# Kernel tuning notes

Hardware: AMD Instinct MI355X
Metric: run time of the kernel (lower is better)

Reference implementation:

```python
import jax, jax.numpy as jnp
import numpy as np

B, L, DM, H, DK, DV = 4, 1024, 1024, 16, 64, 64


def setup_inputs() -> dict:
    key = jax.random.key(0)
    ks = jax.random.split(key, 9)
    s = 0.02
    q = jax.random.normal(ks[0], (B, L, DM), jnp.float32)
    k = jax.random.normal(ks[1], (B, L, DM), jnp.float32)
    v = jax.random.normal(ks[2], (B, L, DM), jnp.float32)
    # causal mask: True = masked out
    attn_mask = jnp.broadcast_to(jnp.triu(jnp.ones((L, L), bool), k=1), (B, L, L))
    w_q = jax.random.normal(ks[3], (DM, H * DK), jnp.float32) * s
    w_k = jax.random.normal(ks[4], (DM, H * DK), jnp.float32) * s
    w_v = jax.random.normal(ks[5], (DM, H * DV), jnp.float32) * s
    w_o = jax.random.normal(ks[6], (H * DV, DM), jnp.float32) * s
    ln_g = jnp.ones((DM,), jnp.float32)
    ln_b = jnp.zeros((DM,), jnp.float32)
    return {"q": q, "k": k, "v": v, "w_q": w_q, "w_k": w_k, "w_v": w_v,
            "w_o": w_o, "ln_g": ln_g, "ln_b": ln_b,
            "attn_mask": attn_mask, "n_head": H}


def _mha(q, k, v, w_q, w_k, w_v, w_o, ln_g, ln_b, attn_mask, n_head):
    b, lq, dm = q.shape
    lk = k.shape[1]
    d_k = w_q.shape[1] // n_head
    d_v = w_v.shape[1] // n_head
    temper = jnp.asarray(np.sqrt(dm), q.dtype)  # NOTE: sqrt(d_model), as in source
    residual = q
    # faithful to source: flat .view reshape (b, l, h*d) -> (b*h, l, d), NO transpose
    qh = (q @ w_q).reshape(b * n_head, lq, d_k)
    kh = (k @ w_k).reshape(b * n_head, lk, d_k)
    vh = (v @ w_v).reshape(b * n_head, lk, d_v)
    attn = jnp.einsum('bqd,bkd->bqk', qh, kh) / temper  # (b*h, lq, lk)
    mask_r = jnp.tile(attn_mask, (n_head, 1, 1))
    attn = jnp.where(mask_r, -jnp.inf, attn)
    attn = jax.nn.softmax(attn, axis=-1)
    out = jnp.einsum('bqk,bkd->bqd', attn, vh)  # (b*h, lq, d_v)
    out = out.reshape(b, lq, n_head * d_v)
    out = out @ w_o + residual  # dropout = identity (eval)
    mu = jnp.mean(out, axis=-1, keepdims=True)
    var = jnp.mean(jnp.square(out - mu), axis=-1, keepdims=True)
    out = (out - mu) * jax.lax.rsqrt(var + 1e-6) * ln_g + ln_b
    return out, attn


def reference(q, k, v, w_q, w_k, w_v, w_o, ln_g, ln_b, attn_mask, n_head):
    return _mha(q, k, v, w_q, w_k, w_v, w_o, ln_g, ln_b, attn_mask, n_head)
```

## Files before the change

kernel.cpp:

```cpp
#include <hip/hip_runtime.h>
#include <stdint.h>

typedef unsigned short u16;
typedef __attribute__((ext_vector_type(8))) short bf16x8;
typedef __attribute__((ext_vector_type(4))) float f32x4;
typedef __attribute__((ext_vector_type(4))) unsigned short us4;

#define MFMA_BF16(a, b, c) __builtin_amdgcn_mfma_f32_16x16x32_bf16((a), (b), (c), 0, 0, 0)

__device__ __forceinline__ u16 f2bf(float f) {
  uint32_t u = __builtin_bit_cast(uint32_t, f);
  u += 0x7fffu + ((u >> 16) & 1u);
  return (u16)(u >> 16);
}

__device__ __forceinline__ void async_copy16(void* lds, const void* g) {
  __builtin_amdgcn_global_load_lds(
      (const __attribute__((address_space(1))) unsigned int*)g,
      (__attribute__((address_space(3))) unsigned int*)lds, 16, 0, 0);
}

__global__ __launch_bounds__(256) void k_pre(const float* __restrict__ q,
                                             const float* __restrict__ k,
                                             const float* __restrict__ v,
                                             const float* __restrict__ w0,
                                             const float* __restrict__ w1,
                                             const float* __restrict__ w2,
                                             const float* __restrict__ w3,
                                             us4* __restrict__ qkvb,
                                             u16* __restrict__ wT) {
  __shared__ float t[32][33];
  int bid = blockIdx.x;
  int tid = threadIdx.x;
  if (bid < 12288) {
    int z = bid >> 12;
    const float4* src = (z == 0) ? (const float4*)q : (z == 1) ? (const float4*)k : (const float4*)v;
    int i = (bid & 4095) * 256 + tid;
    float4 val = src[i];
    us4 o;
    o[0] = f2bf(val.x); o[1] = f2bf(val.y); o[2] = f2bf(val.z); o[3] = f2bf(val.w);
    qkvb[(size_t)z * 1048576 + i] = o;
  } else {
    int w = bid - 12288;
    int z = w >> 10, r_ = w & 1023;
    int bx = r_ & 31, by = r_ >> 5;
    const float* W = (z == 0) ? w0 : (z == 1) ? w1 : (z == 2) ? w2 : w3;
    u16* WT = wT + (size_t)z * 1048576;
    int c = tid & 31, r0 = tid >> 5;
#pragma unroll
    for (int i = 0; i < 4; ++i) {
      int r = r0 + i * 8;
      t[r][c] = W[(size_t)(by * 32 + r) * 1024 + bx * 32 + c];
    }
    __syncthreads();
#pragma unroll
    for (int i = 0; i < 4; ++i) {
      int r = r0 + i * 8;
      WT[(size_t)(bx * 32 + r) * 1024 + by * 32 + c] = f2bf(t[c][r]);
    }
  }
}

__global__ __launch_bounds__(256) void k_vtrans(const u16* __restrict__ VP, u16* __restrict__ VT) {
  int jt = blockIdx.x;
  int bh = blockIdx.y;
  __shared__ u16 t[64][65];
  int tid = threadIdx.x;
  const u16* src = VP + (size_t)bh * 65536 + (size_t)jt * 64 * 64;
#pragma unroll
  for (int i = 0; i < 16; ++i) {
    int e = tid + i * 256;
    t[e >> 6][e & 63] = src[e];
  }
  __syncthreads();
  u16* dst = VT + (size_t)bh * 65536 + jt * 64;
#pragma unroll
  for (int i = 0; i < 16; ++i) {
    int e = tid + i * 256;
    int d = e >> 6, j = e & 63;
    dst[(size_t)d * 1024 + j] = t[j][d];
  }
}

__global__ __launch_bounds__(256) void k_gemm_bt(const u16* __restrict__ A,
                                                 const u16* __restrict__ BT,
                                                 u16* __restrict__ Cb, float* __restrict__ Cf,
                                                 const float* __restrict__ res,
                                                 int N, int K, int mode, int wgrp) {
  __shared__ __align__(16) u16 SM[4][4096];
  int bm, bn;
  {
    int wg = blockIdx.x + blockIdx.y * gridDim.x;
    int per = gridDim.y >> 3;
    int xcd = wg & 7;
    int idx = wg >> 3;
    bm = xcd * per + (idx % per);
    bn = idx / per;
  }
  int tid = threadIdx.x;
  int wave = tid >> 6, lane = tid & 63;
  int wr = wave >> 1, wc = wave & 1;
  int fl = lane & 15, fg = lane >> 4;
  f32x4 acc[4][4] = {};

  const char* Abase = (const char*)(A + (size_t)bm * 128 * K);
  const char* Bbase = (const char*)(BT + (wgrp ? (size_t)(bm >> 5) * 1048576 : 0) +
                                    (size_t)bn * 128 * K);
  int off = wave * 1024 + lane * 16;

#define GSTAGE(buf, kt)                                                              \
  {                                                                                  \
    _Pragma("unroll") for (int is = 0; is < 2; ++is) {                               \
      int o = is * 4096 + off;                                                       \
      int row = o >> 6, cb = o & 63;                                                 \
      async_copy16((char*)SM[buf] + is * 4096 + wave * 1024,                         \
                   Abase + (size_t)row * (K * 2) + (kt) * 2 + cb);                   \
      async_copy16((char*)SM[2 + (buf)] + is * 4096 + wave * 1024,                   \
                   Bbase + (size_t)row * (K * 2) + (kt) * 2 + cb);                   \
    }                                                                                \
  }

  GSTAGE(0, 0);
  __syncthreads();
  int cur = 0;
  for (int kt = 0; kt < K; kt += 32) {
    if (kt + 32 < K) GSTAGE(cur ^ 1, kt + 32);
    bf16x8 af[4], bfr[4];
#pragma unroll
    for (int m = 0; m < 4; ++m)
      af[m] = *(const bf16x8*)((const char*)SM[cur] + (wr * 64 + m * 16 + fl) * 64 + fg * 16);
#pragma unroll
    for (int n = 0; n < 4; ++n)
      bfr[n] = *(const bf16x8*)((const char*)SM[2 + cur] + (wc * 64 + n * 16 + fl) * 64 + fg * 16);
#pragma unroll
    for (int m = 0; m < 4; ++m)
#pragma unroll
      for (int n = 0; n < 4; ++n)
        acc[m][n] = MFMA_BF16(af[m], bfr[n], acc[m][n]);
    __syncthreads();
    cur ^= 1;
  }
#undef GSTAGE

  float* EP = (float*)&SM[0][0] + wave * 2048;
  int colbase = bn * 128 + wc * 64;
#pragma unroll
  for (int m = 0; m < 4; ++m) {
    int rowbase = bm * 128 + wr * 64 + m * 16;
#pragma unroll
    for (int n = 0; n < 4; ++n)
#pragma unroll
      for (int r = 0; r < 4; ++r)
        EP[(fg * 4 + r) * 68 + n * 16 + fl] = acc[m][n][r];
    if (mode) {
#pragma unroll
      for (int j = 0; j < 4; ++j) {
        int row = (lane >> 4) + 4 * j;
        int colf = (lane & 15) * 4;
        float4 val = *(const float4*)(&EP[row * 68 + colf]);
        size_t gidx = (size_t)(rowbase + row) * N + colbase + colf;
        float4 rr = *(const float4*)(res + gidx);
        val.x += rr.x; val.y += rr.y; val.z += rr.z; val.w += rr.w;
        *(float4*)(Cf + gidx) = val;
      }
    } else {
#pragma unroll
      for (int j = 0; j < 2; ++j) {
        int row = (lane >> 3) + 8 * j;
        int colf = (lane & 7) * 8;
        const float* s = &EP[row * 68 + colf];
        us4 lo, hi;
#pragma unroll
        for (int i = 0; i < 4; ++i) { lo[i] = f2bf(s[i]); hi[i] = f2bf(s[4 + i]); }
        u16* d = Cb + (size_t)(rowbase + row) * N + colbase + colf;
        *(us4*)d = lo;
        *(us4*)(d + 4) = hi;
      }
    }
  }
}

__global__ __launch_bounds__(256) void k_attn(const u16* __restrict__ QP,
                                              const u16* __restrict__ KP,
                                              const u16* __restrict__ VT,
                                              float* __restrict__ attn,
                                              u16* __restrict__ AO) {
  int bh = blockIdx.x;
  int qb = 15 - blockIdx.y;
  int tid = threadIdx.x;
  int wave = tid >> 6, lane = tid & 63;
  int fl = lane & 15, fg = lane >> 4;
  int qw = qb * 64 + wave * 16;

  const u16* Qb = QP + (size_t)bh * 65536;
  const char* Kbyte = (const char*)(KP + (size_t)bh * 65536);
  const u16* Vb = VT + (size_t)bh * 65536;
  float* Ab = attn + (size_t)bh * 1048576;

  __shared__ __align__(16) u16 Ks[2][4096];
  __shared__ __align__(16) float Ps[4][16][36];
  __shared__ __align__(16) u16 Pt[4][16][64];

#define KSTAGE(buf, jt)                                                                 \
  {                                                                                     \
    _Pragma("unroll") for (int c2 = 0; c2 < 2; ++c2) {                                  \
      int o = c2 * 4096 + wave * 1024 + lane * 16;                                      \
      int row = o >> 7, col = o & 127;                                                  \
      async_copy16((char*)Ks[buf] + c2 * 4096 + wave * 1024,                            \
                   Kbyte + (size_t)((jt) * 64 + row) * 128 + (col ^ ((row & 7) << 4))); \
    }                                                                                   \
  }

  bf16x8 qf0 = *(const bf16x8*)(Qb + (size_t)(qw + fl) * 64 + fg * 8);
  bf16x8 qf1 = *(const bf16x8*)(Qb + (size_t)(qw + fl) * 64 + 32 + fg * 8);

  float den[4] = {0.f, 0.f, 0.f, 0.f};

  KSTAGE(0, 0);
  __syncthreads();
  int cur = 0;
  for (int jt = 0; jt <= qb; ++jt) {
    if (jt < qb) KSTAGE(cur ^ 1, jt + 1);
    int j0 = jt * 64;
    f32x4 c[4] = {};
#pragma unroll
    for (int n = 0; n < 4; ++n) {
      int r = n * 16 + fl;
      bf16x8 k0 = *(const bf16x8*)((const char*)Ks[cur] + r * 128 + ((fg * 16) ^ ((r & 7) << 4)));
      bf16x8 k1 = *(const bf16x8*)((const char*)Ks[cur] + r * 128 + ((64 + fg * 16) ^ ((r & 7) << 4)));
      c[n] = MFMA_BF16(qf0, k0, c[n]);
      c[n] = MFMA_BF16(qf1, k1, c[n]);
    }
#pragma unroll
    for (int r = 0; r < 4; ++r) {
      int row = qw + fg * 4 + r;
      float sum = 0.f;
#pragma unroll
      for (int n = 0; n < 4; ++n) {
        int col = j0 + n * 16 + fl;
        sum += (col > row) ? 0.f : __expf(c[n][r] * 0.03125f);
      }
#pragma unroll
      for (int o2 = 1; o2 < 16; o2 <<= 1) sum += __shfl_xor(sum, o2);
      den[r] += sum;
    }
    __syncthreads();
    cur ^= 1;
  }

  float invden[4];
#pragma unroll
  for (int r = 0; r < 4; ++r) invden[r] = 1.0f / den[r];

  f32x4 oacc[4] = {};

  KSTAGE(0, 0);
  __syncthreads();
  cur = 0;
  for (int jt = 0; jt <= qb; ++jt) {
    if (jt < qb) KSTAGE(cur ^ 1, jt + 1);
    int j0 = jt * 64;
    f32x4 c[4] = {};
#pragma unroll
    for (int n = 0; n < 4; ++n) {
      int r = n * 16 + fl;
      bf16x8 k0 = *(const bf16x8*)((const char*)Ks[cur] + r * 128 + ((fg * 16) ^ ((r & 7) << 4)));
      bf16x8 k1 = *(const bf16x8*)((const char*)Ks[cur] + r * 128 + ((64 + fg * 16) ^ ((r & 7) << 4)));
      c[n] = MFMA_BF16(qf0, k0, c[n]);
      c[n] = MFMA_BF16(qf1, k1, c[n]);
    }
    float pv_[4][4];
#pragma unroll
    for (int r = 0; r < 4; ++r) {
      int row = qw + fg * 4 + r;
#pragma unroll
      for (int n = 0; n < 4; ++n) {
        int col = j0 + n * 16 + fl;
        pv_[n][r] = (col > row) ? 0.f : __expf(c[n][r] * 0.03125f) * invden[r];
      }
    }
#pragma unroll
    for (int t = 0; t < 2; ++t) {
#pragma unroll
      for (int n2 = 0; n2 < 2; ++n2)
#pragma unroll
        for (int r = 0; r < 4; ++r)
          Ps[wave][fg * 4 + r][n2 * 16 + fl] = pv_[t * 2 + n2][r];
#pragma unroll
      for (int i = 0; i < 2; ++i) {
        int idx = i * 64 + lane;
        int r16 = idx >> 3, f4 = idx & 7;
        float4 val = *(const float4*)(&Ps[wave][r16][f4 * 4]);
        *(float4*)(Ab + (size_t)(qw + r16) * 1024 + j0 + t * 32 + f4 * 4) = val;
      }
    }
#pragma unroll
    for (int r = 0; r < 4; ++r)
#pragma unroll
      for (int n = 0; n < 4; ++n)
        Pt[wave][fg * 4 + r][n * 16 + fl] = f2bf(pv_[n][r]);
    bf16x8 pa0 = *(const bf16x8*)(&Pt[wave][fl][fg * 8]);
    bf16x8 pa1 = *(const bf16x8*)(&Pt[wave][fl][32 + fg * 8]);
#pragma unroll
    for (int n = 0; n < 4; ++n) {
      const u16* vp = Vb + (size_t)(n * 16 + fl) * 1024 + j0;
      bf16x8 v0 = *(const bf16x8*)(vp + fg * 8);
      bf16x8 v1 = *(const bf16x8*)(vp + 32 + fg * 8);
      oacc[n] = MFMA_BF16(pa0, v0, oacc[n]);
      oacc[n] = MFMA_BF16(pa1, v1, oacc[n]);
    }
    __syncthreads();
    cur ^= 1;
  }
#undef KSTAGE

  float4 z; z.x = 0.f; z.y = 0.f; z.z = 0.f; z.w = 0.f;
  for (int jt = qb + 1; jt < 16; ++jt) {
    int j0 = jt * 64;
#pragma unroll
    for (int i = 0; i < 4; ++i) {
      int idx = i * 64 + lane;
      int r16 = idx >> 4, f4 = idx & 15;
      *(float4*)(Ab + (size_t)(qw + r16) * 1024 + j0 + f4 * 4) = z;
    }
  }

#pragma unroll
  for (int n = 0; n < 4; ++n)
#pragma unroll
    for (int r = 0; r < 4; ++r)
      Pt[wave][fg * 4 + r][n * 16 + fl] = f2bf(oacc[n][r]);
#pragma unroll
  for (int j = 0; j < 2; ++j) {
    int row = (lane >> 3) + 8 * j;
    int colf = (lane & 7) * 8;
    bf16x8 val = *(const bf16x8*)(&Pt[wave][row][colf]);
    *(bf16x8*)(AO + (size_t)bh * 65536 + (size_t)(qw + row) * 64 + colf) = val;
  }
}

__global__ __launch_bounds__(256) void k_lnorm(float* __restrict__ io,
                                               const float* __restrict__ g,
                                               const float* __restrict__ b) {
  int row = blockIdx.x, tid = threadIdx.x;
  float* p = io + (size_t)row * 1024 + tid * 4;
  float4 x = *(const float4*)p;
  float s1 = x.x + x.y + x.z + x.w;
  float s2 = x.x * x.x + x.y * x.y + x.z * x.z + x.w * x.w;
#pragma unroll
  for (int o = 1; o < 64; o <<= 1) {
    s1 += __shfl_xor(s1, o);
    s2 += __shfl_xor(s2, o);
  }
  __shared__ float r1[4], r2[4];
  int wave = tid >> 6;
  if ((tid & 63) == 0) { r1[wave] = s1; r2[wave] = s2; }
  __syncthreads();
  s1 = r1[0] + r1[1] + r1[2] + r1[3];
  s2 = r2[0] + r2[1] + r2[2] + r2[3];
  float mu = s1 * (1.0f / 1024.0f);
  float var = s2 * (1.0f / 1024.0f) - mu * mu;
  float rs = rsqrtf(var + 1e-6f);
  float4 gg = *(const float4*)(g + tid * 4);
  float4 bb = *(const float4*)(b + tid * 4);
  float4 y;
  y.x = (x.x - mu) * rs * gg.x + bb.x;
  y.y = (x.y - mu) * rs * gg.y + bb.y;
  y.z = (x.z - mu) * rs * gg.z + bb.z;
  y.w = (x.w - mu) * rs * gg.w + bb.w;
  *(float4*)p = y;
}

extern "C" void kernel_launch(void* const* d_in, const int* in_sizes, int n_in,
                              void* d_out, int out_size, void* d_ws, size_t ws_size,
                              hipStream_t stream) {
  const float* q = (const float*)d_in[0];
  const float* k = (const float*)d_in[1];
  const float* v = (const float*)d_in[2];
  const float* w_q = (const float*)d_in[3];
  const float* w_k = (const float*)d_in[4];
  const float* w_v = (const float*)d_in[5];
  const float* w_o = (const float*)d_in[6];
  const float* ln_g = (const float*)d_in[7];
  const float* ln_b = (const float*)d_in[8];

  float* out = (float*)d_out;
  float* attnp = out + 4194304;

  char* ws = (char*)d_ws;
  u16* QP = (u16*)(ws);
  u16* VP = (u16*)(ws + (16u << 20));
  u16* VT = (u16*)(ws + (24u << 20));
  u16* AO = (u16*)(ws + (32u << 20));
  u16* wT = (u16*)(ws + (40u << 20));
  u16* KP = QP + 4194304;
  u16* woT = wT + 3145728;

  u16* qkvb = (u16*)attnp;

  k_pre<<<16384, 256, 0, stream>>>(q, k, v, w_q, w_k, w_v, w_o, (us4*)qkvb, wT);

  k_gemm_bt<<<dim3(8, 96), 256, 0, stream>>>(qkvb, wT, QP, nullptr, nullptr, 1024, 1024, 0, 1);

  k_vtrans<<<dim3(16, 64), 256, 0, stream>>>(VP, VT);

  k_attn<<<dim3(64, 16), 256, 0, stream>>>(QP, KP, VT, attnp, AO);

  k_gemm_bt<<<dim3(8, 32), 256, 0, stream>>>(AO, woT, nullptr, out, q, 1024, 1024, 1, 0);

  k_lnorm<<<4096, 256, 0, stream>>>(out, ln_g, ln_b);
}
```

Before: 170.5 us.

## Fuse fp32-to-bf16 input conversion into QKV GEMM and move mask zeroing there

Drops the separate q/k/v fp32-to-bf16 conversion pass. The QKV GEMM now stages fp32 activations into swizzled LDS and converts them to bf16 with packed cvt instructions while loading fragments. Extra blocks in the same QKV launch zero the causal upper triangle of the attention output, work that used to be done at the tail of the attention kernel. The attention kernel also stops staging K through LDS and reads K directly from global memory, removing its barriers. In exchange, the GEMM moves twice as many A bytes through LDS, and the attention kernel relies on uncoalesced direct K reads.

```diff
diff --git a/kernel.cpp b/kernel.cpp
--- a/kernel.cpp
+++ b/kernel.cpp
@@ -20,44 +20,37 @@
       (__attribute__((address_space(3))) unsigned int*)lds, 16, 0, 0);
 }
 
-__global__ __launch_bounds__(256) void k_pre(const float* __restrict__ q,
-                                             const float* __restrict__ k,
-                                             const float* __restrict__ v,
-                                             const float* __restrict__ w0,
-                                             const float* __restrict__ w1,
-                                             const float* __restrict__ w2,
-                                             const float* __restrict__ w3,
-                                             us4* __restrict__ qkvb,
-                                             u16* __restrict__ wT) {
+__device__ __forceinline__ bf16x8 cvt8(f32x4 lo, f32x4 hi) {
+  union { bf16x8 v; uint32_t w[4]; } u;
+  asm("v_cvt_pk_bf16_f32 %0, %1, %2" : "=v"(u.w[0]) : "v"(lo[0]), "v"(lo[1]));
+  asm("v_cvt_pk_bf16_f32 %0, %1, %2" : "=v"(u.w[1]) : "v"(lo[2]), "v"(lo[3]));
+  asm("v_cvt_pk_bf16_f32 %0, %1, %2" : "=v"(u.w[2]) : "v"(hi[0]), "v"(hi[1]));
+  asm("v_cvt_pk_bf16_f32 %0, %1, %2" : "=v"(u.w[3]) : "v"(hi[2]), "v"(hi[3]));
+  return u.v;
+}
+
+__global__ __launch_bounds__(256) void k_wtrans4(const float* __restrict__ w0,
+                                                 const float* __restrict__ w1,
+                                                 const float* __restrict__ w2,
+                                                 const float* __restrict__ w3,
+                                                 u16* __restrict__ dstbase) {
+  const float* W = (blockIdx.z == 0) ? w0 : (blockIdx.z == 1) ? w1
+                   : (blockIdx.z == 2) ? w2 : w3;
+  u16* WT = dstbase + (size_t)blockIdx.z * 1048576;
   __shared__ float t[32][33];
-  int bid = blockIdx.x;
+  int bx = blockIdx.x, by = blockIdx.y;
   int tid = threadIdx.x;
-  if (bid < 12288) {
-    int z = bid >> 12;
-    const float4* src = (z == 0) ? (const float4*)q : (z == 1) ? (const float4*)k : (const float4*)v;
-    int i = (bid & 4095) * 256 + tid;
-    float4 val = src[i];
-    us4 o;
-    o[0] = f2bf(val.x); o[1] = f2bf(val.y); o[2] = f2bf(val.z); o[3] = f2bf(val.w);
-    qkvb[(size_t)z * 1048576 + i] = o;
-  } else {
-    int w = bid - 12288;
-    int z = w >> 10, r_ = w & 1023;
-    int bx = r_ & 31, by = r_ >> 5;
-    const float* W = (z == 0) ? w0 : (z == 1) ? w1 : (z == 2) ? w2 : w3;
-    u16* WT = wT + (size_t)z * 1048576;
-    int c = tid & 31, r0 = tid >> 5;
-#pragma unroll
-    for (int i = 0; i < 4; ++i) {
-      int r = r0 + i * 8;
-      t[r][c] = W[(size_t)(by * 32 + r) * 1024 + bx * 32 + c];
-    }
-    __syncthreads();
-#pragma unroll
-    for (int i = 0; i < 4; ++i) {
-      int r = r0 + i * 8;
-      WT[(size_t)(bx * 32 + r) * 1024 + by * 32 + c] = f2bf(t[c][r]);
-    }
+  int c = tid & 31, r0 = tid >> 5;
+#pragma unroll
+  for (int i = 0; i < 4; ++i) {
+    int r = r0 + i * 8;
+    t[r][c] = W[(size_t)(by * 32 + r) * 1024 + bx * 32 + c];
+  }
+  __syncthreads();
+#pragma unroll
+  for (int i = 0; i < 4; ++i) {
+    int r = r0 + i * 8;
+    WT[(size_t)(bx * 32 + r) * 1024 + by * 32 + c] = f2bf(t[c][r]);
   }
 }
 
@@ -82,56 +75,83 @@
   }
 }
 
-__global__ __launch_bounds__(256) void k_gemm_bt(const u16* __restrict__ A,
-                                                 const u16* __restrict__ BT,
-                                                 u16* __restrict__ Cb, float* __restrict__ Cf,
-                                                 const float* __restrict__ res,
-                                                 int N, int K, int mode, int wgrp) {
-  __shared__ __align__(16) u16 SM[4][4096];
-  int bm, bn;
-  {
-    int wg = blockIdx.x + blockIdx.y * gridDim.x;
-    int per = gridDim.y >> 3;
-    int xcd = wg & 7;
-    int idx = wg >> 3;
-    bm = xcd * per + (idx % per);
-    bn = idx / per;
-  }
+__global__ __launch_bounds__(256) void k_gemm_qkv(const float* __restrict__ q,
+                                                  const float* __restrict__ k,
+                                                  const float* __restrict__ v,
+                                                  const u16* __restrict__ wT,
+                                                  u16* __restrict__ C,
+                                                  float* __restrict__ attnp) {
+  __shared__ __align__(16) float Asm[2][4096];
+  __shared__ __align__(16) u16 Bsm[2][4096];
+  int id = blockIdx.x;
+  int xcd = id & 7, seq = id >> 3;
+  int grp = seq / 7, r7 = seq % 7;
   int tid = threadIdx.x;
+  if (r7 >= 3) {
+    int zid = xcd * 128 + grp * 4 + (r7 - 3);
+    int bh = zid >> 4, qb = zid & 15;
+    int W = 960 - 64 * qb;
+    if (W > 0 && tid * 4 < W) {
+      float* base = attnp + (size_t)bh * 1048576 + (size_t)qb * 65536 + (qb + 1) * 64 + tid * 4;
+      float4 z = {0.f, 0.f, 0.f, 0.f};
+#pragma unroll 8
+      for (int row = 0; row < 64; ++row) *(float4*)(base + row * 1024) = z;
+    }
+    return;
+  }
+  int gi = grp * 3 + r7;
+  int bn = gi & 7;
+  int bm = xcd * 12 + (gi >> 3);
+  int z = bm >> 5;
   int wave = tid >> 6, lane = tid & 63;
   int wr = wave >> 1, wc = wave & 1;
   int fl = lane & 15, fg = lane >> 4;
   f32x4 acc[4][4] = {};
 
-  const char* Abase = (const char*)(A + (size_t)bm * 128 * K);
-  const char* Bbase = (const char*)(BT + (wgrp ? (size_t)(bm >> 5) * 1048576 : 0) +
-                                    (size_t)bn * 128 * K);
-  int off = wave * 1024 + lane * 16;
-
-#define GSTAGE(buf, kt)                                                              \
-  {                                                                                  \
-    _Pragma("unroll") for (int is = 0; is < 2; ++is) {                               \
-      int o = is * 4096 + off;                                                       \
-      int row = o >> 6, cb = o & 63;                                                 \
-      async_copy16((char*)SM[buf] + is * 4096 + wave * 1024,                         \
-                   Abase + (size_t)row * (K * 2) + (kt) * 2 + cb);                   \
-      async_copy16((char*)SM[2 + (buf)] + is * 4096 + wave * 1024,                   \
-                   Bbase + (size_t)row * (K * 2) + (kt) * 2 + cb);                   \
-    }                                                                                \
-  }
-
-  GSTAGE(0, 0);
+  const char* Ab = (const char*)((z == 0 ? q : z == 1 ? k : v) + (size_t)(bm & 31) * 131072);
+  const char* Bb = (const char*)(wT + (size_t)z * 1048576 + (size_t)bn * 131072);
+
+#define ASTAGE(buf, kt)                                                        \
+  {                                                                            \
+    _Pragma("unroll") for (int is = 0; is < 4; ++is) {                         \
+      int o = is * 4096 + wave * 1024 + lane * 16;                             \
+      int row = o >> 7, cb = o & 127;                                          \
+      async_copy16((char*)Asm[buf] + is * 4096 + wave * 1024,                  \
+                   Ab + (size_t)row * 4096 + (kt) * 4 + (cb ^ ((row & 7) << 4))); \
+    }                                                                          \
+  }
+#define BSTAGE(buf, kt)                                                        \
+  {                                                                            \
+    _Pragma("unroll") for (int is = 0; is < 2; ++is) {                         \
+      int o = is * 4096 + wave * 1024 + lane * 16;                             \
+      int row = o >> 6, cb = o & 63;                                           \
+      async_copy16((char*)Bsm[buf] + is * 4096 + wave * 1024,                  \
+                   Bb + (size_t)row * 2048 + (kt) * 2 + cb);                   \
+    }                                                                          \
+  }
+
+  ASTAGE(0, 0);
+  BSTAGE(0, 0);
   __syncthreads();
   int cur = 0;
-  for (int kt = 0; kt < K; kt += 32) {
-    if (kt + 32 < K) GSTAGE(cur ^ 1, kt + 32);
+  for (int kt = 0; kt < 1024; kt += 32) {
+    if (kt + 32 < 1024) {
+      ASTAGE(cur ^ 1, kt + 32);
+      BSTAGE(cur ^ 1, kt + 32);
+    }
     bf16x8 af[4], bfr[4];
 #pragma unroll
-    for (int m = 0; m < 4; ++m)
-      af[m] = *(const bf16x8*)((const char*)SM[cur] + (wr * 64 + m * 16 + fl) * 64 + fg * 16);
+    for (int m = 0; m < 4; ++m) {
+      int R = wr * 64 + m * 16 + fl;
+      const char* ar = (const char*)Asm[cur] + R * 128;
+      int s = (R & 7) << 4;
+      f32x4 lo = *(const f32x4*)(ar + ((fg * 32) ^ s));
+      f32x4 hi = *(const f32x4*)(ar + ((fg * 32 + 16) ^ s));
+      af[m] = cvt8(lo, hi);
+    }
 #pragma unroll
     for (int n = 0; n < 4; ++n)
-      bfr[n] = *(const bf16x8*)((const char*)SM[2 + cur] + (wc * 64 + n * 16 + fl) * 64 + fg * 16);
+      bfr[n] = *(const bf16x8*)((const char*)Bsm[cur] + (wc * 64 + n * 16 + fl) * 64 + fg * 16);
 #pragma unroll
     for (int m = 0; m < 4; ++m)
 #pragma unroll
@@ -140,9 +160,10 @@
     __syncthreads();
     cur ^= 1;
   }
-#undef GSTAGE
-
-  float* EP = (float*)&SM[0][0] + wave * 2048;
+#undef ASTAGE
+#undef BSTAGE
+
+  float* EP = (float*)&Asm[0][0] + wave * 1088;
   int colbase = bn * 128 + wc * 64;
 #pragma unroll
   for (int m = 0; m < 4; ++m) {
@@ -152,30 +173,17 @@
 #pragma unroll
       for (int r = 0; r < 4; ++r)
         EP[(fg * 4 + r) * 68 + n * 16 + fl] = acc[m][n][r];
-    if (mode) {
-#pragma unroll
-      for (int j = 0; j < 4; ++j) {
-        int row = (lane >> 4) + 4 * j;
-        int colf = (lane & 15) * 4;
-        float4 val = *(const float4*)(&EP[row * 68 + colf]);
-        size_t gidx = (size_t)(rowbase + row) * N + colbase + colf;
-        float4 rr = *(const float4*)(res + gidx);
-        val.x += rr.x; val.y += rr.y; val.z += rr.z; val.w += rr.w;
-        *(float4*)(Cf + gidx) = val;
-      }
-    } else {
-#pragma unroll
-      for (int j = 0; j < 2; ++j) {
-        int row = (lane >> 3) + 8 * j;
-        int colf = (lane & 7) * 8;
-        const float* s = &EP[row * 68 + colf];
-        us4 lo, hi;
-#pragma unroll
-        for (int i = 0; i < 4; ++i) { lo[i] = f2bf(s[i]); hi[i] = f2bf(s[4 + i]); }
-        u16* d = Cb + (size_t)(rowbase + row) * N + colbase + colf;
-        *(us4*)d = lo;
-        *(us4*)(d + 4) = hi;
-      }
+#pragma unroll
+    for (int j = 0; j < 2; ++j) {
+      int row = (lane >> 3) + 8 * j;
+      int colf = (lane & 7) * 8;
+      const float* sp = &EP[row * 68 + colf];
+      us4 lo4, hi4;
+#pragma unroll
+      for (int i = 0; i < 4; ++i) { lo4[i] = f2bf(sp[i]); hi4[i] = f2bf(sp[4 + i]); }
+      u16* d = C + (size_t)(rowbase + row) * 1024 + colbase + colf;
+      *(us4*)d = lo4;
+      *(us4*)(d + 4) = hi4;
     }
   }
 }
@@ -193,41 +201,26 @@
   int qw = qb * 64 + wave * 16;
 
   const u16* Qb = QP + (size_t)bh * 65536;
-  const char* Kbyte = (const char*)(KP + (size_t)bh * 65536);
+  const u16* Kb = KP + (size_t)bh * 65536;
   const u16* Vb = VT + (size_t)bh * 65536;
   float* Ab = attn + (size_t)bh * 1048576;
 
-  __shared__ __align__(16) u16 Ks[2][4096];
   __shared__ __align__(16) float Ps[4][16][36];
   __shared__ __align__(16) u16 Pt[4][16][64];
 
-#define KSTAGE(buf, jt)                                                                 \
-  {                                                                                     \
-    _Pragma("unroll") for (int c2 = 0; c2 < 2; ++c2) {                                  \
-      int o = c2 * 4096 + wave * 1024 + lane * 16;                                      \
-      int row = o >> 7, col = o & 127;                                                  \
-      async_copy16((char*)Ks[buf] + c2 * 4096 + wave * 1024,                            \
-                   Kbyte + (size_t)((jt) * 64 + row) * 128 + (col ^ ((row & 7) << 4))); \
-    }                                                                                   \
-  }
-
   bf16x8 qf0 = *(const bf16x8*)(Qb + (size_t)(qw + fl) * 64 + fg * 8);
   bf16x8 qf1 = *(const bf16x8*)(Qb + (size_t)(qw + fl) * 64 + 32 + fg * 8);
 
   float den[4] = {0.f, 0.f, 0.f, 0.f};
 
-  KSTAGE(0, 0);
-  __syncthreads();
-  int cur = 0;
   for (int jt = 0; jt <= qb; ++jt) {
-    if (jt < qb) KSTAGE(cur ^ 1, jt + 1);
     int j0 = jt * 64;
     f32x4 c[4] = {};
 #pragma unroll
     for (int n = 0; n < 4; ++n) {
-      int r = n * 16 + fl;
-      bf16x8 k0 = *(const bf16x8*)((const char*)Ks[cur] + r * 128 + ((fg * 16) ^ ((r & 7) << 4)));
-      bf16x8 k1 = *(const bf16x8*)((const char*)Ks[cur] + r * 128 + ((64 + fg * 16) ^ ((r & 7) << 4)));
+      const u16* kp = Kb + (size_t)(j0 + n * 16 + fl) * 64;
+      bf16x8 k0 = *(const bf16x8*)(kp + fg * 8);
+      bf16x8 k1 = *(const bf16x8*)(kp + 32 + fg * 8);
       c[n] = MFMA_BF16(qf0, k0, c[n]);
       c[n] = MFMA_BF16(qf1, k1, c[n]);
     }
@@ -244,8 +237,6 @@
       for (int o2 = 1; o2 < 16; o2 <<= 1) sum += __shfl_xor(sum, o2);
       den[r] += sum;
     }
-    __syncthreads();
-    cur ^= 1;
   }
 
   float invden[4];
@@ -254,18 +245,14 @@
 
   f32x4 oacc[4] = {};
 
-  KSTAGE(0, 0);
-  __syncthreads();
-  cur = 0;
   for (int jt = 0; jt <= qb; ++jt) {
-    if (jt < qb) KSTAGE(cur ^ 1, jt + 1);
     int j0 = jt * 64;
     f32x4 c[4] = {};
 #pragma unroll
     for (int n = 0; n < 4; ++n) {
-      int r = n * 16 + fl;
-      bf16x8 k0 = *(const bf16x8*)((const char*)Ks[cur] + r * 128 + ((fg * 16) ^ ((r & 7) << 4)));
-      bf16x8 k1 = *(const bf16x8*)((const char*)Ks[cur] + r * 128 + ((64 + fg * 16) ^ ((r & 7) << 4)));
+      const u16* kp = Kb + (size_t)(j0 + n * 16 + fl) * 64;
+      bf16x8 k0 = *(const bf16x8*)(kp + fg * 8);
+      bf16x8 k1 = *(const bf16x8*)(kp + 32 + fg * 8);
       c[n] = MFMA_BF16(qf0, k0, c[n]);
       c[n] = MFMA_BF16(qf1, k1, c[n]);
     }
@@ -309,20 +296,6 @@
       oacc[n] = MFMA_BF16(pa0, v0, oacc[n]);
       oacc[n] = MFMA_BF16(pa1, v1, oacc[n]);
     }
-    __syncthreads();
-    cur ^= 1;
-  }
-#undef KSTAGE
-
-  float4 z; z.x = 0.f; z.y = 0.f; z.z = 0.f; z.w = 0.f;
-  for (int jt = qb + 1; jt < 16; ++jt) {
-    int j0 = jt * 64;
-#pragma unroll
-    for (int i = 0; i < 4; ++i) {
-      int idx = i * 64 + lane;
-      int r16 = idx >> 4, f4 = idx & 15;
-      *(float4*)(Ab + (size_t)(qw + r16) * 1024 + j0 + f4 * 4) = z;
-    }
   }
 
 #pragma unroll
@@ -336,6 +309,85 @@
     int colf = (lane & 7) * 8;
     bf16x8 val = *(const bf16x8*)(&Pt[wave][row][colf]);
     *(bf16x8*)(AO + (size_t)bh * 65536 + (size_t)(qw + row) * 64 + colf) = val;
+  }
+}
+
+__global__ __launch_bounds__(256) void k_gemm_out(const u16* __restrict__ A,
+                                                  const u16* __restrict__ BT,
+                                                  float* __restrict__ Cf,
+                                                  const float* __restrict__ res) {
+  __shared__ __align__(16) u16 SM[4][4096];
+  int bm, bn;
+  {
+    int wg = blockIdx.x + blockIdx.y * 8;
+    int xcd = wg & 7, idx = wg >> 3;
+    bm = xcd * 4 + (idx & 3);
+    bn = idx >> 2;
+  }
+  int tid = threadIdx.x;
+  int wave = tid >> 6, lane = tid & 63;
+  int wr = wave >> 1, wc = wave & 1;
+  int fl = lane & 15, fg = lane >> 4;
+  f32x4 acc[4][4] = {};
+
+  const char* Abase = (const char*)(A + (size_t)bm * 131072);
+  const char* Bbase = (const char*)(BT + (size_t)bn * 131072);
+  int off = wave * 1024 + lane * 16;
+
+#define GSTAGE(buf, kt)                                                        \
+  {                                                                            \
+    _Pragma("unroll") for (int is = 0; is < 2; ++is) {                         \
+      int o = is * 4096 + off;                                                 \
+      int row = o >> 6, cb = o & 63;                                           \
+      async_copy16((char*)SM[buf] + is * 4096 + wave * 1024,                   \
+                   Abase + (size_t)row * 2048 + (kt) * 2 + cb);                \
+      async_copy16((char*)SM[2 + (buf)] + is * 4096 + wave * 1024,             \
+                   Bbase + (size_t)row * 2048 + (kt) * 2 + cb);                \
+    }                                                                          \
+  }
+
+  GSTAGE(0, 0);
+  __syncthreads();
+  int cur = 0;
+  for (int kt = 0; kt < 1024; kt += 32) {
+    if (kt + 32 < 1024) GSTAGE(cur ^ 1, kt + 32);
+    bf16x8 af[4], bfr[4];
+#pragma unroll
+    for (int m = 0; m < 4; ++m)
+      af[m] = *(const bf16x8*)((const char*)SM[cur] + (wr * 64 + m * 16 + fl) * 64 + fg * 16);
+#pragma unroll
+    for (int n = 0; n < 4; ++n)
+      bfr[n] = *(const bf16x8*)((const char*)SM[2 + cur] + (wc * 64 + n * 16 + fl) * 64 + fg * 16);
+#pragma unroll
+    for (int m = 0; m < 4; ++m)
+#pragma unroll
+      for (int n = 0; n < 4; ++n)
+        acc[m][n] = MFMA_BF16(af[m], bfr[n], acc[m][n]);
+    __syncthreads();
+    cur ^= 1;
+  }
+#undef GSTAGE
+
+  float* EP = (float*)&SM[0][0] + wave * 1088;
+  int colbase = bn * 128 + wc * 64;
+#pragma unroll
+  for (int m = 0; m < 4; ++m) {
+    int rowbase = bm * 128 + wr * 64 + m * 16;
+#pragma unroll
+    for (int n = 0; n < 4; ++n)
+#pragma unroll
+      for (int r = 0; r < 4; ++r)
+        EP[(fg * 4 + r) * 68 + n * 16 + fl] = acc[m][n][r];
+#pragma unroll
+    for (int j = 0; j < 4; ++j) {
+      int row = (lane >> 4) + 4 * j;
+      int colf = (lane & 15) * 4;
+      float4 val = *(const float4*)(&EP[row * 68 + colf]);
+      size_t gidx = (size_t)(rowbase + row) * 1024 + colbase + colf;
+      float4 rr = *(const float4*)(res + gidx);
+      val.x += rr.x; val.y += rr.y; val.z += rr.z; val.w += rr.w;
+      *(float4*)(Cf + gidx) = val;
+    }
   }
 }
 
@@ -389,24 +441,22 @@
 
   char* ws = (char*)d_ws;
   u16* QP = (u16*)(ws);
+  u16* KP = QP + 4194304;
   u16* VP = (u16*)(ws + (16u << 20));
   u16* VT = (u16*)(ws + (24u << 20));
   u16* AO = (u16*)(ws + (32u << 20));
   u16* wT = (u16*)(ws + (40u << 20));
-  u16* KP = QP + 4194304;
   u16* woT = wT + 3145728;
 
-  u16* qkvb = (u16*)attnp;
-
-  k_pre<<<16384, 256, 0, stream>>>(q, k, v, w_q, w_k, w_v, w_o, (us4*)qkvb, wT);
-
-  k_gemm_bt<<<dim3(8, 96), 256, 0, stream>>>(qkvb, wT, QP, nullptr, nullptr, 1024, 1024, 0, 1);
+  k_wtrans4<<<dim3(32, 32, 4), 256, 0, stream>>>(w_q, w_k, w_v, w_o, wT);
+
+  k_gemm_qkv<<<1792, 256, 0, stream>>>(q, k, v, wT, QP, attnp);
 
   k_vtrans<<<dim3(16, 64), 256, 0, stream>>>(VP, VT);
 
   k_attn<<<dim3(64, 16), 256, 0, stream>>>(QP, KP, VT, attnp, AO);
 
-  k_gemm_bt<<<dim3(8, 32), 256, 0, stream>>>(AO, woT, nullptr, out, q, 1024, 1024, 1, 0);
+  k_gemm_out<<<dim3(8, 32), 256, 0, stream>>>(AO, woT, out, q);
 
   k_lnorm<<<4096, 256, 0, stream>>>(out, ln_g, ln_b);
 }
```

Measured after the change: 256.7 us. 50.6% more time.
